# Kernel tuning notes

Hardware: AMD Instinct MI355X
Metric: run time of the kernel (lower is better)

Reference implementation:

```python
import jax, jax.numpy as jnp
import numpy as np

N_TRUCK = 100000
N_CAR = 100000
E = 1600000
H = 128
P = 200000


def _gcn(x, edge_index, edge_weight, W, b, num_nodes):
    """PyG GCNConv: D^{-1/2}(A+I)D^{-1/2} x W + b with self-loop weight 1."""
    h = x @ W  # [N, H]
    row, col = edge_index[0], edge_index[1]
    deg = jax.ops.segment_sum(edge_weight, col, num_segments=num_nodes) + 1.0  # +1 self-loop
    dis = jax.lax.rsqrt(deg)
    norm = dis[row] * edge_weight * dis[col]  # [E]
    agg = jax.ops.segment_sum(norm[:, None] * h[row], col, num_segments=num_nodes)
    agg = agg + (dis * dis)[:, None] * h  # self-loop contribution
    return agg + b


def setup_inputs() -> dict:
    key = jax.random.key(0)
    ks = jax.random.split(key, 12)
    return {
        "x_car": jax.random.normal(ks[0], (N_CAR, 3), dtype=jnp.float32),
        "edge_index_truck": jax.random.randint(ks[1], (2, E), 0, N_TRUCK, dtype=jnp.int64)
        if jax.config.jax_enable_x64 else jax.random.randint(ks[1], (2, E), 0, N_TRUCK, dtype=jnp.int32),
        "edge_index_car": jax.random.randint(ks[2], (2, E), 0, N_CAR, dtype=jnp.int32),
        "edge_weight_car": jax.random.uniform(ks[3], (E,), dtype=jnp.float32),
        "src": jax.random.randint(ks[4], (P,), 0, N_TRUCK + N_CAR, dtype=jnp.int32),
        "dst": jax.random.randint(ks[5], (P,), 0, N_TRUCK + N_CAR, dtype=jnp.int32),
        "n_truck": N_TRUCK,
        "W_truck": jax.random.normal(ks[6], (1, H), dtype=jnp.float32) * 0.5,
        "b_truck": jax.random.normal(ks[7], (H,), dtype=jnp.float32) * 0.1,
        "W_car": jax.random.normal(ks[8], (3, H), dtype=jnp.float32) * 0.5,
        "b_car": jax.random.normal(ks[9], (H,), dtype=jnp.float32) * 0.1,
        "W_lin": jax.random.normal(ks[10], (H, 1), dtype=jnp.float32) * 0.1,
        "b_lin": jax.random.normal(ks[11], (1,), dtype=jnp.float32) * 0.1,
    }


def reference(x_car, edge_index_truck, edge_index_car, edge_weight_car,
              src, dst, n_truck, W_truck, b_truck, W_car, b_car, W_lin, b_lin):
    x_truck_in = jnp.ones((n_truck, 1), dtype=x_car.dtype)
    ew_truck = jnp.ones((edge_index_truck.shape[1],), dtype=x_car.dtype)
    h_truck = _gcn(x_truck_in, edge_index_truck, ew_truck, W_truck, b_truck, n_truck)
    h_car = _gcn(x_car, edge_index_car, edge_weight_car, W_car, b_car, x_car.shape[0])
    x = jnp.concatenate([h_truck, h_car], axis=0)  # [N_truck+N_car, H]
    score = (x[src] * x[dst]) @ W_lin + b_lin  # [P, 1]
    return score
```

## Files before the change

### kernel.cpp

```cpp
#include <hip/hip_runtime.h>

typedef unsigned long long u64;

#define N_TRUCK 100000
#define BLK 256
#define NB 128
#define NPB 782
#define CAP 16384
#define PB 256
#define BLK_P 1024
#define CHUNK_MAX 6272
#define ROW_MASK 0x1FFFFu
#define LC_SHIFT 17

#define WS_NEED_NEW 27969920ULL


__global__ void k_place(const int* __restrict__ trow, const int* __restrict__ tcol,
                        const int* __restrict__ crow, const int* __restrict__ ccol,
                        const float* __restrict__ ew, int E_,
                        int* __restrict__ curT, int* __restrict__ curC,
                        unsigned* __restrict__ pT, u64* __restrict__ pC8,
                        const float* __restrict__ Wt, const float* __restrict__ bt,
                        const float* __restrict__ Wc, const float* __restrict__ bc,
                        const float* __restrict__ wlin, float* __restrict__ G) {
    if (blockIdx.x == PB) {
        int l = threadIdx.x;
        if (l < 64) {
            float acc[21];
#pragma unroll
            for (int k = 0; k < 21; k++) acc[k] = 0.0f;
            for (int h = l; h < 128; h += 64) {
                float m[6] = {Wt[h], bt[h], Wc[h], Wc[128 + h], Wc[256 + h], bc[h]};
                float w = wlin[h];
                int k = 0;
#pragma unroll
                for (int a = 0; a < 6; a++)
#pragma unroll
                    for (int b2 = a; b2 < 6; b2++)
                        acc[k++] += m[a] * m[b2] * w;
            }
            int k = 0;
#pragma unroll
            for (int a = 0; a < 6; a++)
#pragma unroll
                for (int b2 = a; b2 < 6; b2++) {
                    float v = acc[k++];
#pragma unroll
                    for (int off = 32; off; off >>= 1) v += __shfl_down(v, off);
                    if (l == 0) {
                        G[a * 6 + b2] = v;
                        G[b2 * 6 + a] = v;
                    }
                }
        }
        return;
    }

    __shared__ u64 pay8[CHUNK_MAX];
    __shared__ unsigned char bkt[CHUNK_MAX];
    __shared__ int hist[NB];
    __shared__ int shiftA[NB];
    unsigned* pay4 = (unsigned*)pay8;

    int b = blockIdx.x;
    int chunk = (E_ + PB - 1) / PB;
    int s0 = b * chunk, s1 = min(E_, s0 + chunk);
    int n = s1 - s0;
    int t = threadIdx.x;

    for (int k = t; k < NB; k += BLK_P) hist[k] = 0;
    __syncthreads();
    for (int j = s0 + t; j < s1; j += BLK_P) atomicAdd(&hist[tcol[j] / NPB], 1);
    __syncthreads();
    int myCnt = (t < NB) ? hist[t] : 0;
    if (t < NB) shiftA[t] = myCnt;
    __syncthreads();
    for (int off = 1; off < NB; off <<= 1) {
        int x = (t < NB && t >= off) ? shiftA[t - off] : 0;
        __syncthreads();
        if (t < NB) shiftA[t] += x;
        __syncthreads();
    }
    if (t < NB) {
        int excl = shiftA[t] - myCnt;
        int gstart = t * CAP + atomicAdd(&curT[t], myCnt);
        shiftA[t] = gstart - excl;
        hist[t] = excl;
    }
    __syncthreads();
    for (int j = s0 + t; j < s1; j += BLK_P) {
        int tc = tcol[j];
        int k = tc / NPB;
        int s = atomicAdd(&hist[k], 1);
        pay4[s] = ((unsigned)(tc - k * NPB) << LC_SHIFT) | (unsigned)trow[j];
        bkt[s] = (unsigned char)k;
    }
    __syncthreads();
    for (int s = t; s < n; s += BLK_P)
        pT[s + shiftA[bkt[s]]] = pay4[s];
    __syncthreads();

    for (int k = t; k < NB; k += BLK_P) hist[k] = 0;
    __syncthreads();
    for (int j = s0 + t; j < s1; j += BLK_P) atomicAdd(&hist[ccol[j] / NPB], 1);
    __syncthreads();
    myCnt = (t < NB) ? hist[t] : 0;
    if (t < NB) shiftA[t] = myCnt;
    __syncthreads();
    for (int off = 1; off < NB; off <<= 1) {
        int x = (t < NB && t >= off) ? shiftA[t - off] : 0;
        __syncthreads();
        if (t < NB) shiftA[t] += x;
        __syncthreads();
    }
    if (t < NB) {
        int excl = shiftA[t] - myCnt;
        int gstart = t * CAP + atomicAdd(&curC[t], myCnt);
        shiftA[t] = gstart - excl;
        hist[t] = excl;
    }
    __syncthreads();
    for (int j = s0 + t; j < s1; j += BLK_P) {
        int cc = ccol[j];
        int k = cc / NPB;
        int s = atomicAdd(&hist[k], 1);
        unsigned lo = ((unsigned)(cc - k * NPB) << LC_SHIFT) | (unsigned)crow[j];
        pay8[s] = ((u64)__float_as_uint(ew[j]) << 32) | lo;
        bkt[s] = (unsigned char)k;
    }
    __syncthreads();
    for (int s = t; s < n; s += BLK_P)
        pC8[s + shiftA[bkt[s]]] = pay8[s];
}


__global__ void k_deg2(const unsigned* __restrict__ pT, const u64* __restrict__ pC8,
                       const int* __restrict__ curT, const int* __restrict__ curC,
                       float* __restrict__ dis_t, float* __restrict__ dis_c,
                       int nt, int nc) {
    __shared__ float acc[NPB];
    int b = blockIdx.x;
    bool car = b >= NB;
    int bk = car ? b - NB : b;
    int cnt = car ? curC[bk] : curT[bk];
    int s0 = bk * CAP;
    for (int k = threadIdx.x; k < NPB; k += blockDim.x) acc[k] = 0.0f;
    __syncthreads();
    if (car) {
        for (int j = threadIdx.x; j < cnt; j += blockDim.x) {
            u64 v = pC8[s0 + j];
            atomicAdd(&acc[((unsigned)v) >> LC_SHIFT], __uint_as_float((unsigned)(v >> 32)));
        }
    } else {
        for (int j = threadIdx.x; j < cnt; j += blockDim.x)
            atomicAdd(&acc[pT[s0 + j] >> LC_SHIFT], 1.0f);
    }
    __syncthreads();
    float* dis = car ? dis_c : dis_t;
    int ntot = car ? nc : nt;
    for (int nn = threadIdx.x; nn < NPB; nn += blockDim.x) {
        int node = bk * NPB + nn;
        if (node < ntot) dis[node] = rsqrtf(acc[nn] + 1.0f);
    }
}


__global__ void k_agg(const unsigned* __restrict__ pT, const u64* __restrict__ pC8,
                      const int* __restrict__ curT, const int* __restrict__ curC,
                      const float* __restrict__ dis_t, const float* __restrict__ dis_c,
                      const float* __restrict__ x_car,
                      float* __restrict__ s_t, float4* __restrict__ y4,
                      int nt, int nc) {
    int b = blockIdx.x;
    if (b < NB) {
        __shared__ float sacc[NPB];
        int cnt = curT[b];
        int s0 = b * CAP;
        for (int k = threadIdx.x; k < NPB; k += blockDim.x) sacc[k] = 0.0f;
        __syncthreads();
        for (int j = threadIdx.x; j < cnt; j += blockDim.x) {
            unsigned v = pT[s0 + j];
            atomicAdd(&sacc[v >> LC_SHIFT], dis_t[v & ROW_MASK]);
        }
        __syncthreads();
        for (int nn = threadIdx.x; nn < NPB; nn += blockDim.x) {
            int node = b * NPB + nn;
            if (node < nt) {
                float d = dis_t[node];
                s_t[node] = fmaf(d, sacc[nn], d * d);
            }
        }
    } else {
        int bk = b - NB;
        __shared__ float y[NPB * 5];
        __shared__ float dcl[NPB];
        int cnt = curC[bk];
        int s0 = bk * CAP;
        for (int k = threadIdx.x; k < NPB * 5; k += blockDim.x) y[k] = 0.0f;
        for (int k = threadIdx.x; k < NPB; k += blockDim.x) {
            int node = bk * NPB + k;
            dcl[k] = (node < nc) ? dis_c[node] : 0.0f;
        }
        __syncthreads();
        for (int j = threadIdx.x; j < cnt; j += blockDim.x) {
            u64 v = pC8[s0 + j];
            int r = (int)((unsigned)v & ROW_MASK);
            int lc = (int)(((unsigned)v) >> LC_SHIFT);
            float nrm = dis_c[r] * __uint_as_float((unsigned)(v >> 32)) * dcl[lc];
            const float* xr = &x_car[3 * r];
            atomicAdd(&y[lc * 5 + 0], nrm * xr[0]);
            atomicAdd(&y[lc * 5 + 1], nrm * xr[1]);
            atomicAdd(&y[lc * 5 + 2], nrm * xr[2]);
        }
        __syncthreads();
        for (int nn = threadIdx.x; nn < NPB; nn += blockDim.x) {
            int node = bk * NPB + nn;
            if (node < nc) {
                float d2 = dcl[nn] * dcl[nn];
                const float* xn = &x_car[3 * node];
                y4[node] = make_float4(fmaf(d2, xn[0], y[nn * 5 + 0]),
                                       fmaf(d2, xn[1], y[nn * 5 + 1]),
                                       fmaf(d2, xn[2], y[nn * 5 + 2]), 1.0f);
            }
        }
    }
}


__device__ __forceinline__ void load_z(int i, const float* __restrict__ s_t,
                                       const float4* __restrict__ y4, float z[6]) {
    if (i < N_TRUCK) {
        z[0] = s_t[i]; z[1] = 1.0f; z[2] = 0.0f; z[3] = 0.0f; z[4] = 0.0f; z[5] = 0.0f;
    } else {
        float4 y = y4[i - N_TRUCK];
        z[0] = 0.0f; z[1] = 0.0f; z[2] = y.x; z[3] = y.y; z[4] = y.z; z[5] = 1.0f;
    }
}

__global__ void k_pairs(const int* __restrict__ src, const int* __restrict__ dst, int P_,
                        const float* __restrict__ s_t, const float4* __restrict__ y4,
                        const float* __restrict__ G, const float* __restrict__ b_lin,
                        float* __restrict__ out) {
    int p = blockIdx.x * blockDim.x + threadIdx.x;
    if (p >= P_) return;
    float zs[6], zd[6];
    load_z(src[p], s_t, y4, zs);
    load_z(dst[p], s_t, y4, zd);
    float acc = 0.0f;
#pragma unroll
    for (int a = 0; a < 6; a++) {
        float g = 0.0f;
#pragma unroll
        for (int b = 0; b < 6; b++) g = fmaf(G[a * 6 + b], zd[b], g);
        acc = fmaf(zs[a], g, acc);
    }
    out[p] = acc + b_lin[0];
}


__global__ void k_G(const float* __restrict__ Wt, const float* __restrict__ bt,
                    const float* __restrict__ Wc, const float* __restrict__ bc,
                    const float* __restrict__ wlin, float* __restrict__ G) {
    int l = threadIdx.x;
    float acc[21];
#pragma unroll
    for (int k = 0; k < 21; k++) acc[k] = 0.0f;
    for (int h = l; h < 128; h += 64) {
        float m[6] = {Wt[h], bt[h], Wc[h], Wc[128 + h], Wc[256 + h], bc[h]};
        float w = wlin[h];
        int k = 0;
#pragma unroll
        for (int a = 0; a < 6; a++)
#pragma unroll
            for (int b = a; b < 6; b++)
                acc[k++] += m[a] * m[b] * w;
    }
    int k = 0;
#pragma unroll
    for (int a = 0; a < 6; a++)
#pragma unroll
        for (int b = a; b < 6; b++) {
            float v = acc[k++];
#pragma unroll
            for (int off = 32; off; off >>= 1) v += __shfl_down(v, off);
            if (l == 0) {
                G[a * 6 + b] = v;
                G[b * 6 + a] = v;
            }
        }
}

__global__ void k_deg(const int* __restrict__ tcol, const int* __restrict__ ccol,
                      const float* __restrict__ ew, int E_,
                      int* __restrict__ cnt_t, float* __restrict__ degw_c) {
    int i = blockIdx.x * blockDim.x + threadIdx.x;
    if (i >= E_) return;
    atomicAdd(&cnt_t[tcol[i]], 1);
    atomicAdd(&degw_c[ccol[i]], ew[i]);
}

__global__ void k_dis(const int* __restrict__ cnt_t, const float* __restrict__ degw_c,
                      float* __restrict__ dis_t, float* __restrict__ dis_c,
                      int nt, int nc) {
    int i = blockIdx.x * blockDim.x + threadIdx.x;
    if (i < nt) dis_t[i] = rsqrtf((float)cnt_t[i] + 1.0f);
    if (i < nc) dis_c[i] = rsqrtf(degw_c[i] + 1.0f);
}

__global__ void k_scat(const int* __restrict__ trow, const int* __restrict__ tcol,
                       const int* __restrict__ crow, const int* __restrict__ ccol,
                       const float* __restrict__ ew, int E_,
                       const float* __restrict__ dis_t, const float* __restrict__ dis_c,
                       const float* __restrict__ x_car,
                       float* __restrict__ sumdis, float* __restrict__ y4) {
    int i = blockIdx.x * blockDim.x + threadIdx.x;
    if (i >= E_) return;
    atomicAdd(&sumdis[tcol[i]], dis_t[trow[i]]);
    int r = crow[i], c = ccol[i];
    float nrm = dis_c[r] * ew[i] * dis_c[c];
    atomicAdd(&y4[c * 4 + 0], nrm * x_car[r * 3 + 0]);
    atomicAdd(&y4[c * 4 + 1], nrm * x_car[r * 3 + 1]);
    atomicAdd(&y4[c * 4 + 2], nrm * x_car[r * 3 + 2]);
}

__global__ void k_fin(int nt, int nc,
                      const float* __restrict__ dis_t, const float* __restrict__ sumdis,
                      float* __restrict__ s_t,
                      const float* __restrict__ dis_c, const float* __restrict__ x_car,
                      float* __restrict__ y4) {
    int i = blockIdx.x * blockDim.x + threadIdx.x;
    if (i < nt) {
        float d = dis_t[i];
        s_t[i] = d * sumdis[i] + d * d;
    }
    if (i < nc) {
        float d2 = dis_c[i] * dis_c[i];
        y4[i * 4 + 0] += d2 * x_car[i * 3 + 0];
        y4[i * 4 + 1] += d2 * x_car[i * 3 + 1];
        y4[i * 4 + 2] += d2 * x_car[i * 3 + 2];
        y4[i * 4 + 3] = 1.0f;
    }
}


extern "C" void kernel_launch(void* const* d_in, const int* in_sizes, int n_in,
                              void* d_out, int out_size, void* d_ws, size_t ws_size,
                              hipStream_t stream) {
    const float* x_car  = (const float*)d_in[0];
    const int*   ei_t   = (const int*)d_in[1];
    const int*   ei_c   = (const int*)d_in[2];
    const float* ew_c   = (const float*)d_in[3];
    const int*   src    = (const int*)d_in[4];
    const int*   dst    = (const int*)d_in[5];
    const float* W_t    = (const float*)d_in[7];
    const float* b_t    = (const float*)d_in[8];
    const float* W_c    = (const float*)d_in[9];
    const float* b_c    = (const float*)d_in[10];
    const float* W_lin  = (const float*)d_in[11];
    const float* b_lin  = (const float*)d_in[12];
    float* out = (float*)d_out;

    const int NC = in_sizes[0] / 3;
    const int E_ = in_sizes[1] / 2;
    const int P_ = in_sizes[4];

    const int* trow = ei_t;  const int* tcol = ei_t + E_;
    const int* crow = ei_c;  const int* ccol = ei_c + E_;

    char* ws = (char*)d_ws;
    int gP = (P_ + BLK - 1) / BLK;
    int chunk = (E_ + PB - 1) / PB;

    if (ws_size >= WS_NEED_NEW && chunk <= CHUNK_MAX && NB * NPB >= N_TRUCK &&
        NB * NPB >= NC && NB * CAP >= E_ + 16384) {
        int*      curT  = (int*)(ws + 0);
        int*      curC  = (int*)(ws + 512);
        float*    G     = (float*)(ws + 1024);
        float*    dis_t = (float*)(ws + 4096);
        float*    dis_c = (float*)(ws + 404096);
        float*    s_t   = (float*)(ws + 804096);
        float*    y4    = (float*)(ws + 1204096);
        unsigned* pT    = (unsigned*)(ws + 2804096);
        u64*      pC8   = (u64*)(ws + 11192704);

        hipMemsetAsync(ws, 0, 1024, stream);
        k_place<<<PB + 1, BLK_P, 0, stream>>>(trow, tcol, crow, ccol, ew_c, E_,
                                              curT, curC, pT, pC8,
                                              W_t, b_t, W_c, b_c, W_lin, G);
        k_deg2<<<2 * NB, BLK_P, 0, stream>>>(pT, pC8, curT, curC, dis_t, dis_c,
                                             N_TRUCK, NC);
        k_agg<<<2 * NB, BLK_P, 0, stream>>>(pT, pC8, curT, curC, dis_t, dis_c,
                                            x_car, s_t, (float4*)y4, N_TRUCK, NC);
        k_pairs<<<gP, BLK, 0, stream>>>(src, dst, P_, s_t, (const float4*)y4, G, b_lin, out);
    } else {
        int*   cnt_t  = (int*)(ws + 0);
        float* sumdis = (float*)(ws + 400000);
        float* degw_c = (float*)(ws + 800000);
        float* y4    = (float*)(ws + 1200000);
        float* dis_t  = (float*)(ws + 2800000);
        float* dis_c  = (float*)(ws + 3200000);
        float* s_t    = (float*)(ws + 3600000);
        float* G      = (float*)(ws + 4000000);

        hipMemsetAsync(ws, 0, 2800000, stream);
        int gE = (E_ + BLK - 1) / BLK;
        int gN = ((N_TRUCK > NC ? N_TRUCK : NC) + BLK - 1) / BLK;
        k_deg<<<gE, BLK, 0, stream>>>(tcol, ccol, ew_c, E_, cnt_t, degw_c);
        k_dis<<<gN, BLK, 0, stream>>>(cnt_t, degw_c, dis_t, dis_c, N_TRUCK, NC);
        k_scat<<<gE, BLK, 0, stream>>>(trow, tcol, crow, ccol, ew_c, E_,
                                       dis_t, dis_c, x_car, sumdis, y4);
        k_fin<<<gN, BLK, 0, stream>>>(N_TRUCK, NC, dis_t, sumdis, s_t, dis_c, x_car, y4);
        k_G<<<1, 64, 0, stream>>>(W_t, b_t, W_c, b_c, W_lin, G);
        k_pairs<<<gP, BLK, 0, stream>>>(src, dst, P_, s_t, (const float4*)y4, G, b_lin, out);
    }
}
```

Measured before the change: 196.4 us.

## Double bucket count, prescale car features by dis, and vectorize payload loads

Doubles the number of destination buckets: smaller per-bucket capacity, more placement blocks, and more blocks in the degree and aggregation kernels, which spreads the work across more compute units. k_deg2 now also writes a float4 of x_car premultiplied by dis_c, so the car aggregation does one aligned 16-byte gather per edge instead of a dis_c gather plus three scalar x_car loads. Bucket payloads are read two at a time with vector loads, and a single thread handles the odd tail. The cost is extra workspace for the float4 table and one extra write pass in k_deg2.

```diff
diff --git a/kernel.cpp b/kernel.cpp
--- a/kernel.cpp
+++ b/kernel.cpp
@@ -4,16 +4,16 @@
 
 #define N_TRUCK 100000
 #define BLK 256
-#define NB 128
-#define NPB 782
-#define CAP 16384
-#define PB 256
+#define NB 256
+#define NPB 391
+#define CAP 8192
+#define PB 512
 #define BLK_P 1024
-#define CHUNK_MAX 6272
+#define CHUNK_MAX 3136
 #define ROW_MASK 0x1FFFFu
 #define LC_SHIFT 17
 
-#define WS_NEED_NEW 27969920ULL
+#define WS_NEED_NEW 29569920ULL
 
 
 __global__ void k_place(const int* __restrict__ trow, const int* __restrict__ tcol,
@@ -137,8 +137,9 @@
 
 __global__ void k_deg2(const unsigned* __restrict__ pT, const u64* __restrict__ pC8,
                        const int* __restrict__ curT, const int* __restrict__ curC,
+                       const float* __restrict__ x_car,
                        float* __restrict__ dis_t, float* __restrict__ dis_c,
-                       int nt, int nc) {
+                       float4* __restrict__ xs4, int nt, int nc) {
     __shared__ float acc[NPB];
     int b = blockIdx.x;
     bool car = b >= NB;
@@ -148,20 +149,42 @@
     for (int k = threadIdx.x; k < NPB; k += blockDim.x) acc[k] = 0.0f;
     __syncthreads();
     if (car) {
-        for (int j = threadIdx.x; j < cnt; j += blockDim.x) {
-            u64 v = pC8[s0 + j];
+        const ulonglong2* p2 = (const ulonglong2*)(pC8 + s0);
+        int half = cnt >> 1;
+        for (int j = threadIdx.x; j < half; j += blockDim.x) {
+            ulonglong2 v = p2[j];
+            atomicAdd(&acc[((unsigned)v.x) >> LC_SHIFT], __uint_as_float((unsigned)(v.x >> 32)));
+            atomicAdd(&acc[((unsigned)v.y) >> LC_SHIFT], __uint_as_float((unsigned)(v.y >> 32)));
+        }
+        if ((cnt & 1) && threadIdx.x == 0) {
+            u64 v = pC8[s0 + cnt - 1];
             atomicAdd(&acc[((unsigned)v) >> LC_SHIFT], __uint_as_float((unsigned)(v >> 32)));
         }
     } else {
-        for (int j = threadIdx.x; j < cnt; j += blockDim.x)
-            atomicAdd(&acc[pT[s0 + j] >> LC_SHIFT], 1.0f);
-    }
-    __syncthreads();
-    float* dis = car ? dis_c : dis_t;
+        const uint2* p2 = (const uint2*)(pT + s0);
+        int half = cnt >> 1;
+        for (int j = threadIdx.x; j < half; j += blockDim.x) {
+            uint2 v = p2[j];
+            atomicAdd(&acc[v.x >> LC_SHIFT], 1.0f);
+            atomicAdd(&acc[v.y >> LC_SHIFT], 1.0f);
+        }
+        if ((cnt & 1) && threadIdx.x == 0)
+            atomicAdd(&acc[pT[s0 + cnt - 1] >> LC_SHIFT], 1.0f);
+    }
+    __syncthreads();
     int ntot = car ? nc : nt;
     for (int nn = threadIdx.x; nn < NPB; nn += blockDim.x) {
         int node = bk * NPB + nn;
-        if (node < ntot) dis[node] = rsqrtf(acc[nn] + 1.0f);
+        if (node < ntot) {
+            float d = rsqrtf(acc[nn] + 1.0f);
+            if (car) {
+                dis_c[node] = d;
+                const float* xn = &x_car[3 * node];
+                xs4[node] = make_float4(d * xn[0], d * xn[1], d * xn[2], d);
+            } else {
+                dis_t[node] = d;
+            }
+        }
     }
 }
 
@@ -169,7 +192,7 @@
 __global__ void k_agg(const unsigned* __restrict__ pT, const u64* __restrict__ pC8,
                       const int* __restrict__ curT, const int* __restrict__ curC,
                       const float* __restrict__ dis_t, const float* __restrict__ dis_c,
-                      const float* __restrict__ x_car,
+                      const float4* __restrict__ xs4,
                       float* __restrict__ s_t, float4* __restrict__ y4,
                       int nt, int nc) {
     int b = blockIdx.x;
@@ -179,8 +202,17 @@
         int s0 = b * CAP;
         for (int k = threadIdx.x; k < NPB; k += blockDim.x) sacc[k] = 0.0f;
         __syncthreads();
-        for (int j = threadIdx.x; j < cnt; j += blockDim.x) {
-            unsigned v = pT[s0 + j];
+        const uint2* p2 = (const uint2*)(pT + s0);
+        int half = cnt >> 1;
+        for (int j = threadIdx.x; j < half; j += blockDim.x) {
+            uint2 v = p2[j];
+            float da = dis_t[v.x & ROW_MASK];
+            float db = dis_t[v.y & ROW_MASK];
+            atomicAdd(&sacc[v.x >> LC_SHIFT], da);
+            atomicAdd(&sacc[v.y >> LC_SHIFT], db);
+        }
+        if ((cnt & 1) && threadIdx.x == 0) {
+            unsigned v = pT[s0 + cnt - 1];
             atomicAdd(&sacc[v >> LC_SHIFT], dis_t[v & ROW_MASK]);
         }
         __syncthreads();
@@ -203,25 +235,42 @@
             dcl[k] = (node < nc) ? dis_c[node] : 0.0f;
         }
         __syncthreads();
-        for (int j = threadIdx.x; j < cnt; j += blockDim.x) {
-            u64 v = pC8[s0 + j];
-            int r = (int)((unsigned)v & ROW_MASK);
-            int lc = (int)(((unsigned)v) >> LC_SHIFT);
-            float nrm = dis_c[r] * __uint_as_float((unsigned)(v >> 32)) * dcl[lc];
-            const float* xr = &x_car[3 * r];
-            atomicAdd(&y[lc * 5 + 0], nrm * xr[0]);
-            atomicAdd(&y[lc * 5 + 1], nrm * xr[1]);
-            atomicAdd(&y[lc * 5 + 2], nrm * xr[2]);
+        const ulonglong2* p2 = (const ulonglong2*)(pC8 + s0);
+        int half = cnt >> 1;
+        for (int j = threadIdx.x; j < half; j += blockDim.x) {
+            ulonglong2 v = p2[j];
+            unsigned loa = (unsigned)v.x, lob = (unsigned)v.y;
+            float4 xa = xs4[loa & ROW_MASK];
+            float4 xb = xs4[lob & ROW_MASK];
+            int lca = loa >> LC_SHIFT, lcb = lob >> LC_SHIFT;
+            float na = __uint_as_float((unsigned)(v.x >> 32)) * dcl[lca];
+            float nb = __uint_as_float((unsigned)(v.y >> 32)) * dcl[lcb];
+            atomicAdd(&y[lca * 5 + 0], na * xa.x);
+            atomicAdd(&y[lca * 5 + 1], na * xa.y);
+            atomicAdd(&y[lca * 5 + 2], na * xa.z);
+            atomicAdd(&y[lcb * 5 + 0], nb * xb.x);
+            atomicAdd(&y[lcb * 5 + 1], nb * xb.y);
+            atomicAdd(&y[lcb * 5 + 2], nb * xb.z);
+        }
+        if ((cnt & 1) && threadIdx.x == 0) {
+            u64 v = pC8[s0 + cnt - 1];
+            unsigned lo = (unsigned)v;
+            float4 xa = xs4[lo & ROW_MASK];
+            int lc = lo >> LC_SHIFT;
+            float na = __uint_as_float((unsigned)(v >> 32)) * dcl[lc];
+            atomicAdd(&y[lc * 5 + 0], na * xa.x);
+            atomicAdd(&y[lc * 5 + 1], na * xa.y);
+            atomicAdd(&y[lc * 5 + 2], na * xa.z);
         }
         __syncthreads();
         for (int nn = threadIdx.x; nn < NPB; nn += blockDim.x) {
             int node = bk * NPB + nn;
             if (node < nc) {
-                float d2 = dcl[nn] * dcl[nn];
-                const float* xn = &x_car[3 * node];
-                y4[node] = make_float4(fmaf(d2, xn[0], y[nn * 5 + 0]),
-                                       fmaf(d2, xn[1], y[nn * 5 + 1]),
-                                       fmaf(d2, xn[2], y[nn * 5 + 2]), 1.0f);
+                float d = dcl[nn];
+                float4 xs = xs4[node];
+                y4[node] = make_float4(fmaf(d, xs.x, y[nn * 5 + 0]),
+                                       fmaf(d, xs.y, y[nn * 5 + 1]),
+                                       fmaf(d, xs.z, y[nn * 5 + 2]), 1.0f);
             }
         }
     }
@@ -373,31 +422,32 @@
     int chunk = (E_ + PB - 1) / PB;
 
     if (ws_size >= WS_NEED_NEW && chunk <= CHUNK_MAX && NB * NPB >= N_TRUCK &&
-        NB * NPB >= NC && NB * CAP >= E_ + 16384) {
+        NB * NPB >= NC && NB * CAP >= E_ + 8192) {
         int*      curT  = (int*)(ws + 0);
-        int*      curC  = (int*)(ws + 512);
-        float*    G     = (float*)(ws + 1024);
+        int*      curC  = (int*)(ws + 1024);
+        float*    G     = (float*)(ws + 2048);
         float*    dis_t = (float*)(ws + 4096);
         float*    dis_c = (float*)(ws + 404096);
         float*    s_t   = (float*)(ws + 804096);
         float*    y4    = (float*)(ws + 1204096);
-        unsigned* pT    = (unsigned*)(ws + 2804096);
-        u64*      pC8   = (u64*)(ws + 11192704);
-
-        hipMemsetAsync(ws, 0, 1024, stream);
+        float4*   xs4   = (float4*)(ws + 2804096);
+        unsigned* pT    = (unsigned*)(ws + 4404096);
+        u64*      pC8   = (u64*)(ws + 12792704);
+
+        hipMemsetAsync(ws, 0, 2048, stream);
         k_place<<<PB + 1, BLK_P, 0, stream>>>(trow, tcol, crow, ccol, ew_c, E_,
                                               curT, curC, pT, pC8,
                                               W_t, b_t, W_c, b_c, W_lin, G);
-        k_deg2<<<2 * NB, BLK_P, 0, stream>>>(pT, pC8, curT, curC, dis_t, dis_c,
-                                             N_TRUCK, NC);
+        k_deg2<<<2 * NB, BLK_P, 0, stream>>>(pT, pC8, curT, curC, x_car,
+                                             dis_t, dis_c, xs4, N_TRUCK, NC);
         k_agg<<<2 * NB, BLK_P, 0, stream>>>(pT, pC8, curT, curC, dis_t, dis_c,
-                                            x_car, s_t, (float4*)y4, N_TRUCK, NC);
+                                            xs4, s_t, (float4*)y4, N_TRUCK, NC);
         k_pairs<<<gP, BLK, 0, stream>>>(src, dst, P_, s_t, (const float4*)y4, G, b_lin, out);
     } else {
         int*   cnt_t  = (int*)(ws + 0);
         float* sumdis = (float*)(ws + 400000);
         float* degw_c = (float*)(ws + 800000);
-        float* y4    = (float*)(ws + 1200000);
+        float* y4     = (float*)(ws + 1200000);
         float* dis_t  = (float*)(ws + 2800000);
         float* dis_c  = (float*)(ws + 3200000);
         float* s_t    = (float*)(ws + 3600000);
```

Result: faster. 184.2 us (-6.2%).
